# Optimization experiments

Hardware: AMD Instinct MI355X
Metric: run time of the kernel (lower is better)

The kernel has to match this reference:

```python
import jax, jax.numpy as jnp
import numpy as np

B, L, D = 16, 4096, 512
WORD_SIZE = 2048  # codebook_size // 4
WORD_LEN = 2


def setup_inputs() -> dict:
    key = jax.random.key(0)
    k1, k2, k3, k4, k5 = jax.random.split(key, 5)
    char_tokens = jax.random.randint(k1, (B, L), 0, 8192, dtype=jnp.int64 if jax.config.jax_enable_x64 else jnp.int32)
    char_embeddings = jax.random.normal(k2, (B, L, D), dtype=jnp.float32)
    # word_codebook initialized uniform(-1/word_size, 1/word_size) in the original
    word_codebook = jax.random.uniform(k3, (WORD_SIZE, D), dtype=jnp.float32,
                                       minval=-1.0 / WORD_SIZE, maxval=1.0 / WORD_SIZE)
    proj_w = jax.random.normal(k4, (D, D), dtype=jnp.float32) * (1.0 / np.sqrt(D))
    proj_b = jax.random.normal(k5, (D,), dtype=jnp.float32) * 0.01
    return {"char_tokens": char_tokens, "char_embeddings": char_embeddings,
            "word_codebook": word_codebook, "proj_w": proj_w, "proj_b": proj_b}


def reference(char_tokens, char_embeddings, word_codebook, proj_w, proj_b):
    Bv, Lv, Dv = char_embeddings.shape
    G = Lv // WORD_LEN  # number of 2-char groups per sequence
    # mean-pool each consecutive pair of characters -> [B, G, D]
    means = char_embeddings.reshape(Bv, G, WORD_LEN, Dv).mean(axis=2)
    # squared-euclidean nearest codebook entry (same argmin as cdist)
    # d2[b,g,k] = ||m||^2 - 2 m.W^T + ||W||^2 ; ||m||^2 constant over k -> drop
    dots = jnp.einsum('bgd,kd->bgk', means, word_codebook)            # [B,G,K]
    cb_sq = jnp.sum(word_codebook * word_codebook, axis=-1)           # [K]
    word_indices = jnp.argmin(cb_sq[None, None, :] - 2.0 * dots, axis=-1)  # [B,G]
    word_embeddings = word_codebook[word_indices]                     # [B,G,D]
    # alignment loss: mse(proj(word_emb), stop_grad(word_emb))
    projected = jnp.einsum('bgd,ed->bge', word_embeddings, proj_w) + proj_b
    target = jax.lax.stop_gradient(word_embeddings)
    alignment_loss = jnp.mean((projected - target) ** 2)
    return (word_indices, word_embeddings, alignment_loss)
```

## Files before the change

kernel.cpp:

```cpp
#include <hip/hip_runtime.h>


#define D_DIM    512
#define K_CODES  2048
#define N_ROWS   32768
#define EPS_GAP  1e-5f
#define LOSS_SCALE (1.0f / 16777216.0f)
#define LDT      40

typedef __attribute__((ext_vector_type(8))) short short8;
typedef __attribute__((ext_vector_type(4))) float f32x4;

__device__ inline unsigned short f32_bf16(float f) {
    unsigned u = __float_as_uint(f);
    u += 0x7FFFu + ((u >> 16) & 1u);
    return (unsigned short)(u >> 16);
}
__device__ inline float bf16_f32(unsigned short h) { return __uint_as_float(((unsigned)h) << 16); }

__device__ inline void merge_cand(float s, int idx, float& v1, int& i1, float& v2, int& i2) {
    if (s < v1 || (s == v1 && idx < i1)) { v2 = v1; i2 = i1; v1 = s; i1 = idx; }
    else if (s < v2 || (s == v2 && idx < i2)) { v2 = s; i2 = idx; }
}

__global__ __launch_bounds__(256, 1)
void cra_pack_stats(const float* __restrict__ cb,
                    const float* __restrict__ W,
                    const float* __restrict__ pb,
                    unsigned short* __restrict__ wsB,
                    float* __restrict__ cb_sq,
                    float* __restrict__ Sk,
                    float* __restrict__ loss_out,
                    int* __restrict__ counter)
{
    __shared__ float cbs[8 * D_DIM];
    __shared__ float red[4 * 8];
    const int tid = threadIdx.x;
    const int c0  = blockIdx.x * 8;

    if (blockIdx.x == 0 && tid == 0) { loss_out[0] = 0.0f; counter[0] = 0; }

    {
        const float4* src = (const float4*)(cb + (size_t)c0 * D_DIM);
        float4* dst = (float4*)cbs;
        #pragma unroll
        for (int k = 0; k < 4; ++k) dst[tid + k * 256] = src[tid + k * 256];
    }
    __syncthreads();

    if (tid < 8) {
        const float* r = cbs + tid * D_DIM;
        float s = 0.f;
        for (int d = 0; d < D_DIM; ++d) s = fmaf(r[d], r[d], s);
        cb_sq[c0 + tid] = s;
    }

    {
        const int row = tid >> 5;
        const int off = (tid & 31) * 16;
        short8 h[2], l[2];
        #pragma unroll
        for (int g = 0; g < 2; ++g)
            #pragma unroll
            for (int e = 0; e < 8; ++e) {
                float f = cbs[row * D_DIM + off + g * 8 + e];
                unsigned short hi = f32_bf16(f);
                h[g][e] = (short)hi;
                l[g][e] = (short)f32_bf16(f - bf16_f32(hi));
            }
        unsigned short* dst = wsB + (size_t)(c0 + row) * 1024 + off;
        *(short8*)(dst)       = h[0];
        *(short8*)(dst + 8)   = h[1];
        *(short8*)(dst + 512) = l[0];
        *(short8*)(dst + 520) = l[1];
    }

    float part[8];
    #pragma unroll
    for (int c = 0; c < 8; ++c) part[c] = 0.f;
    for (int rep = 0; rep < 2; ++rep) {
        const int e = rep * 256 + tid;
        const float4* wrow = (const float4*)(W + (size_t)e * D_DIM);
        float acc[8];
        #pragma unroll
        for (int c = 0; c < 8; ++c) acc[c] = 0.f;
        for (int dq = 0; dq < D_DIM / 4; ++dq) {
            const float4 wv = wrow[dq];
            #pragma unroll
            for (int c = 0; c < 8; ++c) {
                const float4 cv = ((const float4*)(cbs + c * D_DIM))[dq];
                acc[c] += cv.x * wv.x + cv.y * wv.y + cv.z * wv.z + cv.w * wv.w;
            }
        }
        const float bias = pb[e];
        #pragma unroll
        for (int c = 0; c < 8; ++c) {
            const float diff = acc[c] + bias - cbs[c * D_DIM + e];
            part[c] = fmaf(diff, diff, part[c]);
        }
    }
    #pragma unroll
    for (int c = 0; c < 8; ++c) {
        float v = part[c];
        #pragma unroll
        for (int off = 32; off > 0; off >>= 1) v += __shfl_down(v, off, 64);
        if ((tid & 63) == 0) red[(tid >> 6) * 8 + c] = v;
    }
    __syncthreads();
    if (tid < 8)
        Sk[c0 + tid] = red[0 * 8 + tid] + red[1 * 8 + tid] +
                       red[2 * 8 + tid] + red[3 * 8 + tid];
}

__global__ __launch_bounds__(256, 2)
void cra_gemm(const float* __restrict__ ce,
              const unsigned short* __restrict__ wsB,
              const float* __restrict__ cb_sq,
              float4* __restrict__ wsRed)
{
    __shared__ short sMem[4 * 128 * LDT];
    short* sAh = sMem;
    short* sAl = sMem + 128 * LDT;
    short* sBh = sMem + 2 * 128 * LDT;
    short* sBl = sMem + 3 * 128 * LDT;

    const int tid  = threadIdx.x;
    const int colb = blockIdx.x & 15;
    const int mb   = blockIdx.x >> 4;
    const int rowBase = mb * 128;
    const int colBase = colb * 128;
    const int lane = tid & 63;
    const int w    = tid >> 6;
    const int wr     = (w & 1) * 64;
    const int wcHalf = (w >> 1);
    const int wc     = wcHalf * 64;
    const int cid  = lane & 15;
    const int quad = lane >> 4;

    f32x4 acc[4][4];
    #pragma unroll
    for (int i = 0; i < 4; ++i)
        #pragma unroll
        for (int j = 0; j < 4; ++j) acc[i][j] = (f32x4)(0.f);

    const int srow = tid >> 1;
    const int skh  = (tid & 1) * 16;
    const float* a0p = ce + (size_t)(2 * (rowBase + srow)) * D_DIM + skh;
    const float* a1p = a0p + D_DIM;
    const unsigned short* bp = wsB + (size_t)(colBase + srow) * 1024 + skh;

    float4 pA0[4], pA1[4];
    short8 pBh0, pBh1, pBl0, pBl1;

    #pragma unroll
    for (int q = 0; q < 4; ++q) {
        pA0[q] = *(const float4*)(a0p + q * 4);
        pA1[q] = *(const float4*)(a1p + q * 4);
    }
    pBh0 = *(const short8*)(bp);
    pBh1 = *(const short8*)(bp + 8);
    pBl0 = *(const short8*)(bp + 512);
    pBl1 = *(const short8*)(bp + 520);

    #pragma unroll 1
    for (int c = 0; c < 16; ++c) {
        {
            float m[16];
            #pragma unroll
            for (int q = 0; q < 4; ++q) {
                m[q * 4 + 0] = 0.5f * (pA0[q].x + pA1[q].x);
                m[q * 4 + 1] = 0.5f * (pA0[q].y + pA1[q].y);
                m[q * 4 + 2] = 0.5f * (pA0[q].z + pA1[q].z);
                m[q * 4 + 3] = 0.5f * (pA0[q].w + pA1[q].w);
            }
            short8 h[2], l[2];
            #pragma unroll
            for (int g = 0; g < 2; ++g)
                #pragma unroll
                for (int e = 0; e < 8; ++e) {
                    float f = m[g * 8 + e];
                    unsigned short hi = f32_bf16(f);
                    h[g][e] = (short)hi;
                    l[g][e] = (short)f32_bf16(f - bf16_f32(hi));
                }
            *(short8*)&sAh[srow * LDT + skh]     = h[0];
            *(short8*)&sAh[srow * LDT + skh + 8] = h[1];
            *(short8*)&sAl[srow * LDT + skh]     = l[0];
            *(short8*)&sAl[srow * LDT + skh + 8] = l[1];
            *(short8*)&sBh[srow * LDT + skh]     = pBh0;
            *(short8*)&sBh[srow * LDT + skh + 8] = pBh1;
            *(short8*)&sBl[srow * LDT + skh]     = pBl0;
            *(short8*)&sBl[srow * LDT + skh + 8] = pBl1;
        }
        __syncthreads();

        if (c < 15) {
            const int k0 = (c + 1) * 32;
            #pragma unroll
            for (int q = 0; q < 4; ++q) {
                pA0[q] = *(const float4*)(a0p + k0 + q * 4);
                pA1[q] = *(const float4*)(a1p + k0 + q * 4);
            }
            pBh0 = *(const short8*)(bp + k0);
            pBh1 = *(const short8*)(bp + k0 + 8);
            pBl0 = *(const short8*)(bp + k0 + 512);
            pBl1 = *(const short8*)(bp + k0 + 520);
        }

        short8 aF[4], bF[4];
        #pragma unroll
        for (int mi = 0; mi < 4; ++mi) aF[mi] = *(const short8*)&sAh[(wr + mi * 16 + cid) * LDT + quad * 8];
        #pragma unroll
        for (int ni = 0; ni < 4; ++ni) bF[ni] = *(const short8*)&sBh[(wc + ni * 16 + cid) * LDT + quad * 8];
        #pragma unroll
        for (int mi = 0; mi < 4; ++mi)
            #pragma unroll
            for (int ni = 0; ni < 4; ++ni)
                acc[mi][ni] = __builtin_amdgcn_mfma_f32_16x16x32_bf16(aF[mi], bF[ni], acc[mi][ni], 0, 0, 0);
        #pragma unroll
        for (int mi = 0; mi < 4; ++mi) aF[mi] = *(const short8*)&sAl[(wr + mi * 16 + cid) * LDT + quad * 8];
        #pragma unroll
        for (int mi = 0; mi < 4; ++mi)
            #pragma unroll
            for (int ni = 0; ni < 4; ++ni)
                acc[mi][ni] = __builtin_amdgcn_mfma_f32_16x16x32_bf16(aF[mi], bF[ni], acc[mi][ni], 0, 0, 0);
        #pragma unroll
        for (int mi = 0; mi < 4; ++mi) aF[mi] = *(const short8*)&sAh[(wr + mi * 16 + cid) * LDT + quad * 8];
        #pragma unroll
        for (int ni = 0; ni < 4; ++ni) bF[ni] = *(const short8*)&sBl[(wc + ni * 16 + cid) * LDT + quad * 8];
        #pragma unroll
        for (int mi = 0; mi < 4; ++mi)
            #pragma unroll
            for (int ni = 0; ni < 4; ++ni)
                acc[mi][ni] = __builtin_amdgcn_mfma_f32_16x16x32_bf16(aF[mi], bF[ni], acc[mi][ni], 0, 0, 0);
        __syncthreads();
    }

    float cq[4];
    #pragma unroll
    for (int ni = 0; ni < 4; ++ni) cq[ni] = cb_sq[colBase + wc + ni * 16 + cid];

    float4* sRed = (float4*)sMem;
    #pragma unroll
    for (int mi = 0; mi < 4; ++mi) {
        #pragma unroll
        for (int reg = 0; reg < 4; ++reg) {
            float v1 = 3.4e38f, v2 = 3.4e38f;
            int   i1 = 0x7FFFFFFF, i2 = 0x7FFFFFFF;
            #pragma unroll
            for (int ni = 0; ni < 4; ++ni) {
                float s = fmaf(-2.0f, acc[mi][ni][reg], cq[ni]);
                merge_cand(s, colBase + wc + ni * 16 + cid, v1, i1, v2, i2);
            }
            #pragma unroll
            for (int d = 1; d <= 2; d <<= 1) {
                float ov1 = __shfl_xor(v1, d); int oi1 = __shfl_xor(i1, d);
                float ov2 = __shfl_xor(v2, d); int oi2 = __shfl_xor(i2, d);
                merge_cand(ov1, oi1, v1, i1, v2, i2);
                merge_cand(ov2, oi2, v1, i1, v2, i2);
            }
            if ((cid & 3) == 0) {
                int row = wr + mi * 16 + quad * 4 + reg;
                sRed[(row * 2 + wcHalf) * 4 + (cid >> 2)] =
                    make_float4(v1, __int_as_float(i1), v2, __int_as_float(i2));
            }
        }
    }
    __syncthreads();
    if (tid < 128) {
        float v1 = 3.4e38f, v2 = 3.4e38f;
        int   i1 = 0x7FFFFFFF, i2 = 0x7FFFFFFF;
        #pragma unroll
        for (int e = 0; e < 8; ++e) {
            float4 t = sRed[tid * 8 + e];
            merge_cand(t.x, __float_as_int(t.y), v1, i1, v2, i2);
            merge_cand(t.z, __float_as_int(t.w), v1, i1, v2, i2);
        }
        wsRed[(size_t)(rowBase + tid) * 16 + colb] =
            make_float4(v1, __int_as_float(i1), v2, __int_as_float(i2));
    }
}

__global__ __launch_bounds__(256, 1)
void cra_merge(const float4* __restrict__ wsRed,
               const float* __restrict__ Sk,
               float* __restrict__ out_idx,
               float* __restrict__ out_loss,
               int* __restrict__ counter,
               int* __restrict__ flagRow,
               int2* __restrict__ flagI)
{
    __shared__ float sl[256];
    const int tid = threadIdx.x;
    const int r = blockIdx.x * 256 + tid;
    float v1 = 3.4e38f, v2 = 3.4e38f;
    int   i1 = 0x7FFFFFFF, i2 = 0x7FFFFFFF;
    #pragma unroll 4
    for (int cbk = 0; cbk < 16; ++cbk) {
        float4 t = wsRed[(size_t)r * 16 + cbk];
        merge_cand(t.x, __float_as_int(t.y), v1, i1, v2, i2);
        merge_cand(t.z, __float_as_int(t.w), v1, i1, v2, i2);
    }
    out_idx[r] = (float)i1;
    if (v2 - v1 < EPS_GAP) {
        int slot = atomicAdd(counter, 1);
        flagRow[slot] = r;
        flagI[slot] = make_int2(i1, i2);
    }
    sl[tid] = Sk[i1];
    __syncthreads();
    for (int s = 128; s > 0; s >>= 1) { if (tid < s) sl[tid] += sl[tid + s]; __syncthreads(); }
    if (tid == 0) atomicAdd(out_loss, sl[0] * LOSS_SCALE);
}

__global__ __launch_bounds__(256, 1)
void cra_gather(const float* __restrict__ out_idx,
                const float4* __restrict__ cb4,
                float4* __restrict__ out4)
{
    __shared__ int sidx[128];
    const int tid = threadIdx.x;
    const int rb = blockIdx.x * 128;
    if (tid < 128) sidx[tid] = (int)out_idx[rb + tid];
    __syncthreads();
    for (int j = tid; j < 128 * 128; j += 256) {
        int row = j >> 7, q = j & 127;
        out4[(size_t)(rb + row) * 128 + q] = cb4[(size_t)sidx[row] * 128 + q];
    }
}

__global__ __launch_bounds__(256, 1)
void cra_recheck(const float* __restrict__ ce,
                 const float* __restrict__ cb,
                 const float* __restrict__ cb_sq,
                 const float* __restrict__ Sk,
                 const int* __restrict__ counter,
                 const int* __restrict__ flagRow,
                 const int2* __restrict__ flagI,
                 float* __restrict__ out_idx,
                 float4* __restrict__ out4,
                 float* __restrict__ out_loss,
                 const float4* __restrict__ cb4)
{
    __shared__ float rp[8];
    __shared__ int swin;
    const int tid = threadIdx.x;
    const int n = counter[0];
    for (int f = blockIdx.x; f < n; f += 64) {
        const int row = flagRow[f];
        const int2 ii = flagI[f];
        const int d0 = tid * 2;
        float2 x0 = *(const float2*)(ce + (size_t)(2 * row) * D_DIM + d0);
        float2 x1 = *(const float2*)(ce + (size_t)(2 * row) * D_DIM + D_DIM + d0);
        float m0 = 0.5f * (x0.x + x1.x), m1 = 0.5f * (x0.y + x1.y);
        const float* c1 = cb + (size_t)ii.x * D_DIM + d0;
        const float* c2 = cb + (size_t)ii.y * D_DIM + d0;
        float p1 = fmaf(m0, c1[0], m1 * c1[1]);
        float p2 = fmaf(m0, c2[0], m1 * c2[1]);
        #pragma unroll
        for (int off = 32; off > 0; off >>= 1) {
            p1 += __shfl_down(p1, off, 64);
            p2 += __shfl_down(p2, off, 64);
        }
        if ((tid & 63) == 0) { rp[(tid >> 6) * 2] = p1; rp[(tid >> 6) * 2 + 1] = p2; }
        __syncthreads();
        if (tid == 0) {
            float dot1 = rp[0] + rp[2] + rp[4] + rp[6];
            float dot2 = rp[1] + rp[3] + rp[5] + rp[7];
            float s1 = cb_sq[ii.x] - 2.f * dot1;
            float s2 = cb_sq[ii.y] - 2.f * dot2;
            int win = (s2 < s1 || (s2 == s1 && ii.y < ii.x)) ? ii.y : ii.x;
            swin = win;
            if (win != ii.x) {
                out_idx[row] = (float)win;
                atomicAdd(out_loss, (Sk[win] - Sk[ii.x]) * LOSS_SCALE);
            }
        }
        __syncthreads();
        if (swin != ii.x) {
            for (int q = tid; q < 128; q += 256)
                out4[(size_t)row * 128 + q] = cb4[(size_t)swin * 128 + q];
        }
        __syncthreads();
    }
}

extern "C" void kernel_launch(void* const* d_in, const int* in_sizes, int n_in,
                              void* d_out, int out_size, void* d_ws, size_t ws_size,
                              hipStream_t stream)
{
    const float* ce = (const float*)d_in[1];
    const float* cb = (const float*)d_in[2];
    const float* W  = (const float*)d_in[3];
    const float* pb = (const float*)d_in[4];

    char* ws = (char*)d_ws;
    unsigned short* wsB = (unsigned short*)ws;
    float* cb_sq   = (float*)(ws + 4194304);
    float* Sk      = cb_sq + K_CODES;
    int*   flagRow = (int*)(ws + 4194304 + 16384);
    int2*  flagI   = (int2*)(ws + 4194304 + 16384 + 131072);
    int*   counter = (int*)(ws + 4194304 + 16384 + 131072 + 262144);

    float* out_idx  = (float*)d_out;
    float* out_emb  = out_idx + N_ROWS;
    float* out_loss = out_emb + (size_t)N_ROWS * D_DIM;
    float4* wsRed   = (float4*)out_emb;

    cra_pack_stats<<<256, 256, 0, stream>>>(cb, W, pb, wsB, cb_sq, Sk, out_loss, counter);
    cra_gemm<<<4096, 256, 0, stream>>>(ce, wsB, cb_sq, wsRed);
    cra_merge<<<128, 256, 0, stream>>>(wsRed, Sk, out_idx, out_loss, counter, flagRow, flagI);
    cra_gather<<<256, 256, 0, stream>>>(out_idx, (const float4*)cb, (float4*)out_emb);
    cra_recheck<<<64, 256, 0, stream>>>(ce, cb, cb_sq, Sk, counter, flagRow, flagI,
                                        out_idx, (float4*)out_emb, out_loss, (const float4*)cb);
}
```

Baseline: 957.4 us.

## Restructure codebook prep and GEMM with direct-to-LDS B loads and wider tiles

Splits the codebook prep into a bf16 hi/lo packing kernel that writes a pre-tiled layout and a separate projection/loss kernel that spreads work over more blocks and accumulates with atomics. The main GEMM grows to 512 threads with 128x256 tiles, maps blocks to XCDs for locality, and streams B tiles with global_load_lds DMA instead of register staging. The bf16 split now truncates instead of rounding. Partial-result fan-in to the merge halves from 16 to 8 column blocks. Memsets replace in-kernel initialisation, which adds extra launches.

```diff
diff --git a/kernel.cpp b/kernel.cpp
--- a/kernel.cpp
+++ b/kernel.cpp
@@ -6,134 +6,155 @@
 #define N_ROWS   32768
 #define EPS_GAP  1e-5f
 #define LOSS_SCALE (1.0f / 16777216.0f)
-#define LDT      40
 
 typedef __attribute__((ext_vector_type(8))) short short8;
 typedef __attribute__((ext_vector_type(4))) float f32x4;
 
-__device__ inline unsigned short f32_bf16(float f) {
+__device__ __forceinline__ void split_bf16(float f, unsigned short& h, unsigned short& l) {
     unsigned u = __float_as_uint(f);
-    u += 0x7FFFu + ((u >> 16) & 1u);
-    return (unsigned short)(u >> 16);
-}
-__device__ inline float bf16_f32(unsigned short h) { return __uint_as_float(((unsigned)h) << 16); }
-
-__device__ inline void merge_cand(float s, int idx, float& v1, int& i1, float& v2, int& i2) {
+    h = (unsigned short)(u >> 16);
+    float hr = __uint_as_float(u & 0xFFFF0000u);
+    l = (unsigned short)(__float_as_uint(f - hr) >> 16);
+}
+
+__device__ __forceinline__ void dma16(const void* g, void* l) {
+    __builtin_amdgcn_global_load_lds(
+        (const __attribute__((address_space(1))) unsigned int*)g,
+        (__attribute__((address_space(3))) unsigned int*)l, 16, 0, 0);
+}
+
+__device__ __forceinline__ void merge_cand(float s, int idx, float& v1, int& i1, float& v2, int& i2) {
     if (s < v1 || (s == v1 && idx < i1)) { v2 = v1; i2 = i1; v1 = s; i1 = idx; }
     else if (s < v2 || (s == v2 && idx < i2)) { v2 = s; i2 = idx; }
 }
 
 __global__ __launch_bounds__(256, 1)
-void cra_pack_stats(const float* __restrict__ cb,
-                    const float* __restrict__ W,
-                    const float* __restrict__ pb,
-                    unsigned short* __restrict__ wsB,
-                    float* __restrict__ cb_sq,
-                    float* __restrict__ Sk,
-                    float* __restrict__ loss_out,
-                    int* __restrict__ counter)
-{
-    __shared__ float cbs[8 * D_DIM];
-    __shared__ float red[4 * 8];
+void cra_pack(const float* __restrict__ cb,
+              unsigned short* __restrict__ wsBh,
+              unsigned short* __restrict__ wsBl,
+              float* __restrict__ cb_sq)
+{
+    __shared__ float cbs[32 * D_DIM];
     const int tid = threadIdx.x;
-    const int c0  = blockIdx.x * 8;
-
-    if (blockIdx.x == 0 && tid == 0) { loss_out[0] = 0.0f; counter[0] = 0; }
+    const int c0  = blockIdx.x * 32;
 
     {
         const float4* src = (const float4*)(cb + (size_t)c0 * D_DIM);
         float4* dst = (float4*)cbs;
         #pragma unroll
-        for (int k = 0; k < 4; ++k) dst[tid + k * 256] = src[tid + k * 256];
-    }
-    __syncthreads();
-
-    if (tid < 8) {
+        for (int k = 0; k < 16; ++k) dst[tid + k * 256] = src[tid + k * 256];
+    }
+    __syncthreads();
+
+    if (tid < 32) {
         const float* r = cbs + tid * D_DIM;
         float s = 0.f;
         for (int d = 0; d < D_DIM; ++d) s = fmaf(r[d], r[d], s);
         cb_sq[c0 + tid] = s;
     }
 
+    const int row = tid >> 3;
+    const int k   = c0 + row;
+    const int colb = k >> 8;
+    const int pr   = k & 255;
+    const int d0   = (tid & 7) * 64;
+    #pragma unroll
+    for (int g = 0; g < 8; ++g) {
+        const int d = d0 + g * 8;
+        const int cchunk = d >> 5;
+        const int s = d & 31;
+        short8 h8, l8;
+        #pragma unroll
+        for (int e = 0; e < 8; ++e) {
+            unsigned short hh, ll;
+            split_bf16(cbs[row * D_DIM + d + e], hh, ll);
+            h8[e] = (short)hh; l8[e] = (short)ll;
+        }
+        const size_t off = (size_t)colb * 131072 + cchunk * 8192 + pr * 32 + s;
+        *(short8*)(wsBh + off) = h8;
+        *(short8*)(wsBl + off) = l8;
+    }
+}
+
+__global__ __launch_bounds__(256, 1)
+void cra_proj(const float* __restrict__ cb,
+              const float* __restrict__ W,
+              const float* __restrict__ pb,
+              float* __restrict__ Sk)
+{
+    __shared__ float cbs[32 * D_DIM];
+    __shared__ float red[4 * 32];
+    const int tid = threadIdx.x;
+    const int cblock = blockIdx.x >> 2;
+    const int eb     = blockIdx.x & 3;
+    const int c0 = cblock * 32;
+
     {
-        const int row = tid >> 5;
-        const int off = (tid & 31) * 16;
-        short8 h[2], l[2];
-        #pragma unroll
-        for (int g = 0; g < 2; ++g)
-            #pragma unroll
-            for (int e = 0; e < 8; ++e) {
-                float f = cbs[row * D_DIM + off + g * 8 + e];
-                unsigned short hi = f32_bf16(f);
-                h[g][e] = (short)hi;
-                l[g][e] = (short)f32_bf16(f - bf16_f32(hi));
-            }
-        unsigned short* dst = wsB + (size_t)(c0 + row) * 1024 + off;
-        *(short8*)(dst)       = h[0];
-        *(short8*)(dst + 8)   = h[1];
-        *(short8*)(dst + 512) = l[0];
-        *(short8*)(dst + 520) = l[1];
-    }
-
-    float part[8];
-    #pragma unroll
-    for (int c = 0; c < 8; ++c) part[c] = 0.f;
-    for (int rep = 0; rep < 2; ++rep) {
-        const int e = rep * 256 + tid;
-        const float4* wrow = (const float4*)(W + (size_t)e * D_DIM);
-        float acc[8];
-        #pragma unroll
-        for (int c = 0; c < 8; ++c) acc[c] = 0.f;
-        for (int dq = 0; dq < D_DIM / 4; ++dq) {
-            const float4 wv = wrow[dq];
-            #pragma unroll
-            for (int c = 0; c < 8; ++c) {
-                const float4 cv = ((const float4*)(cbs + c * D_DIM))[dq];
-                acc[c] += cv.x * wv.x + cv.y * wv.y + cv.z * wv.z + cv.w * wv.w;
-            }
-        }
-        const float bias = pb[e];
-        #pragma unroll
-        for (int c = 0; c < 8; ++c) {
-            const float diff = acc[c] + bias - cbs[c * D_DIM + e];
-            part[c] = fmaf(diff, diff, part[c]);
-        }
-    }
-    #pragma unroll
-    for (int c = 0; c < 8; ++c) {
-        float v = part[c];
+        const float4* src = (const float4*)(cb + (size_t)c0 * D_DIM);
+        float4* dst = (float4*)cbs;
+        #pragma unroll
+        for (int k = 0; k < 16; ++k) dst[tid + k * 256] = src[tid + k * 256];
+    }
+    __syncthreads();
+
+    const int e  = eb * 128 + (tid >> 1);
+    const int dh = (tid & 1) * 256;
+    float acc[32];
+    #pragma unroll
+    for (int c = 0; c < 32; ++c) acc[c] = 0.f;
+    const float4* wrow = (const float4*)(W + (size_t)e * D_DIM + dh);
+    for (int dq = 0; dq < 64; ++dq) {
+        const float4 wv = wrow[dq];
+        #pragma unroll
+        for (int c = 0; c < 32; ++c) {
+            const float4 cv = *(const float4*)&cbs[c * D_DIM + dh + dq * 4];
+            acc[c] += cv.x * wv.x + cv.y * wv.y + cv.z * wv.z + cv.w * wv.w;
+        }
+    }
+    const float bias = pb[e];
+    const int w = tid >> 6;
+    #pragma unroll
+    for (int c = 0; c < 32; ++c) {
+        const float full = acc[c] + __shfl_xor(acc[c], 1);
+        const float diff = full + bias - cbs[c * D_DIM + e];
+        float v = (tid & 1) ? 0.f : diff * diff;
         #pragma unroll
         for (int off = 32; off > 0; off >>= 1) v += __shfl_down(v, off, 64);
-        if ((tid & 63) == 0) red[(tid >> 6) * 8 + c] = v;
-    }
-    __syncthreads();
-    if (tid < 8)
-        Sk[c0 + tid] = red[0 * 8 + tid] + red[1 * 8 + tid] +
-                       red[2 * 8 + tid] + red[3 * 8 + tid];
-}
-
-__global__ __launch_bounds__(256, 2)
+        if ((tid & 63) == 0) red[w * 32 + c] = v;
+    }
+    __syncthreads();
+    if (tid < 32)
+        atomicAdd(&Sk[c0 + tid],
+                  red[tid] + red[32 + tid] + red[64 + tid] + red[96 + tid]);
+}
+
+__global__ __launch_bounds__(512, 4)
 void cra_gemm(const float* __restrict__ ce,
-              const unsigned short* __restrict__ wsB,
+              const unsigned short* __restrict__ wsBh,
+              const unsigned short* __restrict__ wsBl,
               const float* __restrict__ cb_sq,
               float4* __restrict__ wsRed)
 {
-    __shared__ short sMem[4 * 128 * LDT];
+    __shared__ short sMem[24576];
     short* sAh = sMem;
-    short* sAl = sMem + 128 * LDT;
-    short* sBh = sMem + 2 * 128 * LDT;
-    short* sBl = sMem + 3 * 128 * LDT;
+    short* sAl = sMem + 4096;
+    short* sBh = sMem + 8192;
+    short* sBl = sMem + 16384;
 
     const int tid  = threadIdx.x;
-    const int colb = blockIdx.x & 15;
-    const int mb   = blockIdx.x >> 4;
+    const int bid  = blockIdx.x;
+    const int xcd  = bid & 7;
+    const int slot = bid >> 3;
+    const int mb   = xcd * 32 + (slot >> 3);
+    const int colb = slot & 7;
     const int rowBase = mb * 128;
-    const int colBase = colb * 128;
+    const int colBase = colb * 256;
+
     const int lane = tid & 63;
     const int w    = tid >> 6;
-    const int wr     = (w & 1) * 64;
-    const int wcHalf = (w >> 1);
-    const int wc     = wcHalf * 64;
+    const int wr   = (w & 1) * 64;
+    const int cw   = w >> 1;
+    const int wc   = cw * 64;
     const int cid  = lane & 15;
     const int quad = lane >> 4;
 
@@ -143,91 +164,76 @@
         #pragma unroll
         for (int j = 0; j < 4; ++j) acc[i][j] = (f32x4)(0.f);
 
-    const int srow = tid >> 1;
-    const int skh  = (tid & 1) * 16;
-    const float* a0p = ce + (size_t)(2 * (rowBase + srow)) * D_DIM + skh;
+    const int srow = tid >> 2;
+    const int sA   = (tid & 3) * 8;
+    const float* a0p = ce + (size_t)(2 * (rowBase + srow)) * D_DIM + sA;
     const float* a1p = a0p + D_DIM;
-    const unsigned short* bp = wsB + (size_t)(colBase + srow) * 1024 + skh;
-
-    float4 pA0[4], pA1[4];
-    short8 pBh0, pBh1, pBl0, pBl1;
-
-    #pragma unroll
-    for (int q = 0; q < 4; ++q) {
-        pA0[q] = *(const float4*)(a0p + q * 4);
-        pA1[q] = *(const float4*)(a1p + q * 4);
-    }
-    pBh0 = *(const short8*)(bp);
-    pBh1 = *(const short8*)(bp + 8);
-    pBl0 = *(const short8*)(bp + 512);
-    pBl1 = *(const short8*)(bp + 520);
+
+    const char* gBh = (const char*)wsBh + ((size_t)colb << 18);
+    const char* gBl = (const char*)wsBl + ((size_t)colb << 18);
+    char* lBh = (char*)sBh + w * 2048;
+    char* lBl = (char*)sBl + w * 2048;
+    const int gwoff = w * 2048 + lane * 16;
+
+    float4 pa[4];
+    pa[0] = *(const float4*)(a0p);     pa[1] = *(const float4*)(a0p + 4);
+    pa[2] = *(const float4*)(a1p);     pa[3] = *(const float4*)(a1p + 4);
 
     #pragma unroll 1
     for (int c = 0; c < 16; ++c) {
         {
-            float m[16];
-            #pragma unroll
-            for (int q = 0; q < 4; ++q) {
-                m[q * 4 + 0] = 0.5f * (pA0[q].x + pA1[q].x);
-                m[q * 4 + 1] = 0.5f * (pA0[q].y + pA1[q].y);
-                m[q * 4 + 2] = 0.5f * (pA0[q].z + pA1[q].z);
-                m[q * 4 + 3] = 0.5f * (pA0[q].w + pA1[q].w);
+            const char* gh = gBh + c * 16384 + gwoff;
+            const char* gl = gBl + c * 16384 + gwoff;
+            dma16(gh,        lBh);
+            dma16(gh + 1024, lBh + 1024);
+            dma16(gl,        lBl);
+            dma16(gl + 1024, lBl + 1024);
+        }
+        {
+            float m[8];
+            m[0] = 0.5f * (pa[0].x + pa[2].x); m[1] = 0.5f * (pa[0].y + pa[2].y);
+            m[2] = 0.5f * (pa[0].z + pa[2].z); m[3] = 0.5f * (pa[0].w + pa[2].w);
+            m[4] = 0.5f * (pa[1].x + pa[3].x); m[5] = 0.5f * (pa[1].y + pa[3].y);
+            m[6] = 0.5f * (pa[1].z + pa[3].z); m[7] = 0.5f * (pa[1].w + pa[3].w);
+            short8 h8, l8;
+            #pragma unroll
+            for (int e = 0; e < 8; ++e) {
+                unsigned short hh, ll;
+                split_bf16(m[e], hh, ll);
+                h8[e] = (short)hh; l8[e] = (short)ll;
             }
-            short8 h[2], l[2];
-            #pragma unroll
-            for (int g = 0; g < 2; ++g)
-                #pragma unroll
-                for (int e = 0; e < 8; ++e) {
-                    float f = m[g * 8 + e];
-                    unsigned short hi = f32_bf16(f);
-                    h[g][e] = (short)hi;
-                    l[g][e] = (short)f32_bf16(f - bf16_f32(hi));
-                }
-            *(short8*)&sAh[srow * LDT + skh]     = h[0];
-            *(short8*)&sAh[srow * LDT + skh + 8] = h[1];
-            *(short8*)&sAl[srow * LDT + skh]     = l[0];
-            *(short8*)&sAl[srow * LDT + skh + 8] = l[1];
-            *(short8*)&sBh[srow * LDT + skh]     = pBh0;
-            *(short8*)&sBh[srow * LDT + skh + 8] = pBh1;
-            *(short8*)&sBl[srow * LDT + skh]     = pBl0;
-            *(short8*)&sBl[srow * LDT + skh + 8] = pBl1;
+            *(short8*)&sAh[srow * 32 + sA] = h8;
+            *(short8*)&sAl[srow * 32 + sA] = l8;
         }
         __syncthreads();
 
         if (c < 15) {
             const int k0 = (c + 1) * 32;
-            #pragma unroll
-            for (int q = 0; q < 4; ++q) {
-                pA0[q] = *(const float4*)(a0p + k0 + q * 4);
-                pA1[q] = *(const float4*)(a1p + k0 + q * 4);
-            }
-            pBh0 = *(const short8*)(bp + k0);
-            pBh1 = *(const short8*)(bp + k0 + 8);
-            pBl0 = *(const short8*)(bp + k0 + 512);
-            pBl1 = *(const short8*)(bp + k0 + 520);
+            pa[0] = *(const float4*)(a0p + k0);     pa[1] = *(const float4*)(a0p + k0 + 4);
+            pa[2] = *(const float4*)(a1p + k0);     pa[3] = *(const float4*)(a1p + k0 + 4);
         }
 
         short8 aF[4], bF[4];
         #pragma unroll
-        for (int mi = 0; mi < 4; ++mi) aF[mi] = *(const short8*)&sAh[(wr + mi * 16 + cid) * LDT + quad * 8];
-        #pragma unroll
-        for (int ni = 0; ni < 4; ++ni) bF[ni] = *(const short8*)&sBh[(wc + ni * 16 + cid) * LDT + quad * 8];
+        for (int mi = 0; mi < 4; ++mi) aF[mi] = *(const short8*)&sAh[(wr + mi * 16 + cid) * 32 + quad * 8];
+        #pragma unroll
+        for (int ni = 0; ni < 4; ++ni) bF[ni] = *(const short8*)&sBh[(wc + ni * 16 + cid) * 32 + quad * 8];
         #pragma unroll
         for (int mi = 0; mi < 4; ++mi)
             #pragma unroll
             for (int ni = 0; ni < 4; ++ni)
                 acc[mi][ni] = __builtin_amdgcn_mfma_f32_16x16x32_bf16(aF[mi], bF[ni], acc[mi][ni], 0, 0, 0);
         #pragma unroll
-        for (int mi = 0; mi < 4; ++mi) aF[mi] = *(const short8*)&sAl[(wr + mi * 16 + cid) * LDT + quad * 8];
+        for (int mi = 0; mi < 4; ++mi) aF[mi] = *(const short8*)&sAl[(wr + mi * 16 + cid) * 32 + quad * 8];
         #pragma unroll
         for (int mi = 0; mi < 4; ++mi)
             #pragma unroll
             for (int ni = 0; ni < 4; ++ni)
                 acc[mi][ni] = __builtin_amdgcn_mfma_f32_16x16x32_bf16(aF[mi], bF[ni], acc[mi][ni], 0, 0, 0);
         #pragma unroll
-        for (int mi = 0; mi < 4; ++mi) aF[mi] = *(const short8*)&sAh[(wr + mi * 16 + cid) * LDT + quad * 8];
-        #pragma unroll
-        for (int ni = 0; ni < 4; ++ni) bF[ni] = *(const short8*)&sBl[(wc + ni * 16 + cid) * LDT + quad * 8];
+        for (int mi = 0; mi < 4; ++mi) aF[mi] = *(const short8*)&sAh[(wr + mi * 16 + cid) * 32 + quad * 8];
+        #pragma unroll
+        for (int ni = 0; ni < 4; ++ni) bF[ni] = *(const short8*)&sBl[(wc + ni * 16 + cid) * 32 + quad * 8];
         #pragma unroll
         for (int mi = 0; mi < 4; ++mi)
             #pragma unroll
@@ -249,7 +255,7 @@
             int   i1 = 0x7FFFFFFF, i2 = 0x7FFFFFFF;
             #pragma unroll
             for (int ni = 0; ni < 4; ++ni) {
-                float s = fmaf(-2.0f, acc[mi][ni][reg], cq[ni]);
+                const float s = fmaf(-2.0f, acc[mi][ni][reg], cq[ni]);
                 merge_cand(s, colBase + wc + ni * 16 + cid, v1, i1, v2, i2);
             }
             #pragma unroll
@@ -260,8 +266,8 @@
                 merge_cand(ov2, oi2, v1, i1, v2, i2);
             }
             if ((cid & 3) == 0) {
-                int row = wr + mi * 16 + quad * 4 + reg;
-                sRed[(row * 2 + wcHalf) * 4 + (cid >> 2)] =
+                const int row = wr + mi * 16 + quad * 4 + reg;
+                sRed[(row * 4 + cw) * 4 + (cid >> 2)] =
                     make_float4(v1, __int_as_float(i1), v2, __int_as_float(i2));
             }
         }
@@ -271,12 +277,12 @@
         float v1 = 3.4e38f, v2 = 3.4e38f;
         int   i1 = 0x7FFFFFFF, i2 = 0x7FFFFFFF;
         #pragma unroll
-        for (int e = 0; e < 8; ++e) {
-            float4 t = sRed[tid * 8 + e];
+        for (int e = 0; e < 16; ++e) {
+            const float4 t = sRed[tid * 16 + e];
             merge_cand(t.x, __float_as_int(t.y), v1, i1, v2, i2);
             merge_cand(t.z, __float_as_int(t.w), v1, i1, v2, i2);
         }
-        wsRed[(size_t)(rowBase + tid) * 16 + colb] =
+        wsRed[(size_t)(rowBase + tid) * 8 + colb] =
             make_float4(v1, __int_as_float(i1), v2, __int_as_float(i2));
     }
 }
@@ -295,15 +301,15 @@
     const int r = blockIdx.x * 256 + tid;
     float v1 = 3.4e38f, v2 = 3.4e38f;
     int   i1 = 0x7FFFFFFF, i2 = 0x7FFFFFFF;
-    #pragma unroll 4
-    for (int cbk = 0; cbk < 16; ++cbk) {
-        float4 t = wsRed[(size_t)r * 16 + cbk];
+    #pragma unroll
+    for (int cbk = 0; cbk < 8; ++cbk) {
+        const float4 t = wsRed[(size_t)r * 8 + cbk];
         merge_cand(t.x, __float_as_int(t.y), v1, i1, v2, i2);
         merge_cand(t.z, __float_as_int(t.w), v1, i1, v2, i2);
     }
     out_idx[r] = (float)i1;
     if (v2 - v1 < EPS_GAP) {
-        int slot = atomicAdd(counter, 1);
+        const int slot = atomicAdd(counter, 1);
         flagRow[slot] = r;
         flagI[slot] = make_int2(i1, i2);
     }
@@ -324,7 +330,7 @@
     if (tid < 128) sidx[tid] = (int)out_idx[rb + tid];
     __syncthreads();
     for (int j = tid; j < 128 * 128; j += 256) {
-        int row = j >> 7, q = j & 127;
+        const int row = j >> 7, q = j & 127;
         out4[(size_t)(rb + row) * 128 + q] = cb4[(size_t)sidx[row] * 128 + q];
     }
 }
@@ -350,9 +356,9 @@
         const int row = flagRow[f];
         const int2 ii = flagI[f];
         const int d0 = tid * 2;
-        float2 x0 = *(const float2*)(ce + (size_t)(2 * row) * D_DIM + d0);
-        float2 x1 = *(const float2*)(ce + (size_t)(2 * row) * D_DIM + D_DIM + d0);
-        float m0 = 0.5f * (x0.x + x1.x), m1 = 0.5f * (x0.y + x1.y);
+        const float2 x0 = *(const float2*)(ce + (size_t)(2 * row) * D_DIM + d0);
+        const float2 x1 = *(const float2*)(ce + (size_t)(2 * row) * D_DIM + D_DIM + d0);
+        const float m0 = 0.5f * (x0.x + x1.x), m1 = 0.5f * (x0.y + x1.y);
         const float* c1 = cb + (size_t)ii.x * D_DIM + d0;
         const float* c2 = cb + (size_t)ii.y * D_DIM + d0;
         float p1 = fmaf(m0, c1[0], m1 * c1[1]);
@@ -365,11 +371,11 @@
         if ((tid & 63) == 0) { rp[(tid >> 6) * 2] = p1; rp[(tid >> 6) * 2 + 1] = p2; }
         __syncthreads();
         if (tid == 0) {
-            float dot1 = rp[0] + rp[2] + rp[4] + rp[6];
-            float dot2 = rp[1] + rp[3] + rp[5] + rp[7];
-            float s1 = cb_sq[ii.x] - 2.f * dot1;
-            float s2 = cb_sq[ii.y] - 2.f * dot2;
-            int win = (s2 < s1 || (s2 == s1 && ii.y < ii.x)) ? ii.y : ii.x;
+            const float dot1 = rp[0] + rp[2] + rp[4] + rp[6];
+            const float dot2 = rp[1] + rp[3] + rp[5] + rp[7];
+            const float s1 = cb_sq[ii.x] - 2.f * dot1;
+            const float s2 = cb_sq[ii.y] - 2.f * dot2;
+            const int win = (s2 < s1 || (s2 == s1 && ii.y < ii.x)) ? ii.y : ii.x;
             swin = win;
             if (win != ii.x) {
                 out_idx[row] = (float)win;
@@ -395,9 +401,10 @@
     const float* pb = (const float*)d_in[4];
 
     char* ws = (char*)d_ws;
-    unsigned short* wsB = (unsigned short*)ws;
+    unsigned short* wsBh = (unsigned short*)ws;
+    unsigned short* wsBl = (unsigned short*)(ws + 2097152);
     float* cb_sq   = (float*)(ws + 4194304);
-    float* Sk      = cb_sq + K_CODES;
+    float* Sk      = (float*)(ws + 4194304 + 8192);
     int*   flagRow = (int*)(ws + 4194304 + 16384);
     int2*  flagI   = (int2*)(ws + 4194304 + 16384 + 131072);
     int*   counter = (int*)(ws + 4194304 + 16384 + 131072 + 262144);
@@ -407,8 +414,13 @@
     float* out_loss = out_emb + (size_t)N_ROWS * D_DIM;
     float4* wsRed   = (float4*)out_emb;
 
-    cra_pack_stats<<<256, 256, 0, stream>>>(cb, W, pb, wsB, cb_sq, Sk, out_loss, counter);
-    cra_gemm<<<4096, 256, 0, stream>>>(ce, wsB, cb_sq, wsRed);
+    hipMemsetAsync(Sk, 0, K_CODES * sizeof(float), stream);
+    hipMemsetAsync(counter, 0, sizeof(int), stream);
+    hipMemsetAsync(out_loss, 0, sizeof(float), stream);
+
+    cra_pack<<<64, 256, 0, stream>>>(cb, wsBh, wsBl, cb_sq);
+    cra_proj<<<256, 256, 0, stream>>>(cb, W, pb, Sk);
+    cra_gemm<<<2048, 512, 0, stream>>>(ce, wsBh, wsBl, cb_sq, wsRed);
     cra_merge<<<128, 256, 0, stream>>>(wsRed, Sk, out_idx, out_loss, counter, flagRow, flagI);
     cra_gather<<<256, 256, 0, stream>>>(out_idx, (const float4*)cb, (float4*)out_emb);
     cra_recheck<<<64, 256, 0, stream>>>(ce, cb, cb_sq, Sk, counter, flagRow, flagI,
```

Measured after the change: 950.8 us. Within noise of the previous version (-0.7%).
